# Kernel optimization log

Measured on AMD Instinct MI355X. Metric: run time of the kernel, lower is better.

## Reference

```python
import jax, jax.numpy as jnp
import numpy as np

N, E = 2048, 65536
EMBED, H0, H1 = 64, 128, 128
VOCAB = 625  # 5**k with k=4
SLOPE = 0.01  # F.leaky_relu_ default negative slope


def setup_inputs() -> dict:
    key = jax.random.key(0)
    ks = jax.random.split(key, 20)
    f = jax.random.normal
    return {
        "node_ids": jax.random.randint(ks[0], (N,), 0, VOCAB),
        "edge_index": jax.random.randint(ks[1], (2, E), 0, N),
        "edge_attr": jax.random.uniform(ks[2], (E, 1), dtype=jnp.float32),
        "m": (jax.random.uniform(ks[3], (N, N)) > 0.5).astype(jnp.float32),
        "emb": f(ks[4], (VOCAB, EMBED), dtype=jnp.float32) * 0.1,
        "l0_lin1": f(ks[5], (H0, EMBED + 1), dtype=jnp.float32) * 0.1,
        "l0_lin2": f(ks[6], (H0, H0), dtype=jnp.float32) * 0.1,
        "l0_att_l": f(ks[7], (H0,), dtype=jnp.float32) * 0.1,
        "l0_att_r": f(ks[8], (EMBED,), dtype=jnp.float32) * 0.1,
        "l0_bias": f(ks[9], (H0,), dtype=jnp.float32) * 0.1,
        "l1_lin1": f(ks[10], (H1, H0 + 1), dtype=jnp.float32) * 0.1,
        "l1_lin2": f(ks[11], (H1, H1), dtype=jnp.float32) * 0.1,
        "l1_att_l": f(ks[12], (H1,), dtype=jnp.float32) * 0.1,
        "l1_att_r": f(ks[13], (H0,), dtype=jnp.float32) * 0.1,
        "l1_bias": f(ks[14], (H1,), dtype=jnp.float32) * 0.1,
        "W1": f(ks[15], (20, (EMBED + H0 + H1) * 2), dtype=jnp.float32) * 0.1,
        "b1": f(ks[16], (20,), dtype=jnp.float32) * 0.1,
        "W2": f(ks[17], (20,), dtype=jnp.float32) * 0.1,
        "b2": f(ks[18], (1,), dtype=jnp.float32) * 0.1,
    }


def _segment_softmax(alpha, index, n):
    # numerically-stable softmax over edges grouped by destination node
    amax = jax.ops.segment_max(alpha, index, num_segments=n)
    amax = jnp.where(jnp.isfinite(amax), amax, 0.0)
    e = jnp.exp(alpha - amax[index])
    denom = jax.ops.segment_sum(e, index, num_segments=n)
    return e / (denom[index] + 1e-16)


def _gate_conv(x, src, dst, edge_attr, lin1, lin2, att_l, att_r, bias, n):
    # PyG AttentiveFP GATEConv: message = lin2(leaky_relu(lin1([x_j, e]))) * alpha
    h = jax.nn.leaky_relu(jnp.concatenate([x[src], edge_attr], axis=-1) @ lin1.T, SLOPE)  # [E,out]
    alpha = jax.nn.leaky_relu(h @ att_l + x[dst] @ att_r, SLOPE)  # [E]
    alpha = _segment_softmax(alpha, dst, n)
    msg = (h @ lin2.T) * alpha[:, None]
    return jax.ops.segment_sum(msg, dst, num_segments=n) + bias


def reference(node_ids, edge_index, edge_attr, m, emb,
              l0_lin1, l0_lin2, l0_att_l, l0_att_r, l0_bias,
              l1_lin1, l1_lin2, l1_att_l, l1_att_r, l1_bias,
              W1, b1, W2, b2):
    src, dst = edge_index[0], edge_index[1]
    x = emb[node_ids]  # [N, EMBED]
    h1 = jax.nn.relu(_gate_conv(x, src, dst, edge_attr, l0_lin1, l0_lin2, l0_att_l, l0_att_r, l0_bias, N))
    h2 = jax.nn.relu(_gate_conv(h1, src, dst, edge_attr, l1_lin1, l1_lin2, l1_att_l, l1_att_r, l1_bias, N))
    feat = jnp.concatenate([x, h1, h2], axis=-1)  # [N, C], C = EMBED+H0+H1
    C = feat.shape[-1]
    # 1x1 conv over concat([x_i, x_j]) == split linear: out[c,i,j] = W1[c,:C]@feat[i] + W1[c,C:]@feat[j] + b1[c]
    a = feat @ W1[:, :C].T  # [N, 20] row (i) term
    b = feat @ W1[:, C:].T  # [N, 20] col (j) term
    h = jax.nn.relu(a[:, None, :] + b[None, :, :] + b1)  # [N, N, 20]
    logits = (h @ W2 + b2[0]) * m  # [N, N]; mask multiplies logits as in original
    return jax.nn.softmax(logits, axis=1)
```

## Files before the change

kernel.cpp:

```cpp
#include <hip/hip_runtime.h>
#include <math.h>

#define N 2048
#define E 65536
#define EMBED 64
#define H 128
#define NT 20
#define C3 320
#define CAP 96
#define SLOPE 0.01f

__device__ __forceinline__ float leaky(float x) { return x > 0.f ? x : SLOPE * x; }

__device__ __forceinline__ float wave_sum(float v) {
#pragma unroll
    for (int o = 32; o > 0; o >>= 1) v += __shfl_xor(v, o, 64);
    return v;
}

__global__ __launch_bounds__(256) void k_scatprep(
    const int* __restrict__ ei, const float* __restrict__ eattr,
    int* __restrict__ cursor, int* __restrict__ srcs, float* __restrict__ eas,
    const float* __restrict__ l1_lin1, float* __restrict__ WT1,
    const float* __restrict__ l0_lin2, float* __restrict__ LT0,
    const float* __restrict__ l1_lin2, float* __restrict__ LT1,
    const int* __restrict__ ids, const float* __restrict__ emb,
    const float* __restrict__ l0_lin1,
    float* __restrict__ x, float* __restrict__ A) {
    int b = blockIdx.x;
    int tid = threadIdx.x;
    if (b < 256) {
        int e = b * 256 + tid;
        int d = ei[E + e];
        int pos = atomicAdd(&cursor[d], 1);
        if (pos < CAP) {
            srcs[d * CAP + pos] = ei[e];
            eas[d * CAP + pos] = eattr[e];
        }
    } else if (b < 448) {
        int j = (b - 256) * 256 + tid;
        if (j < 16384) {
            int c = j >> 7, k = j & 127;
            WT1[j] = l1_lin1[k * (H + 1) + c];
        } else if (j < 32768) {
            int jj = j - 16384; int c = jj >> 7, k = jj & 127;
            LT0[jj] = l0_lin2[k * H + c];
        } else {
            int jj = j - 32768; int c = jj >> 7, k = jj & 127;
            LT1[jj] = l1_lin2[k * H + c];
        }
    } else {
        __shared__ float lw[EMBED][130];
        int n0 = (b - 448) * 8;
        for (int j = tid; j < H * (EMBED + 1); j += 256) {
            int k = j / (EMBED + 1), c = j % (EMBED + 1);
            float v = l0_lin1[j];
            if (c < EMBED) lw[c][k] = v;
        }
        for (int idx = tid; idx < 8 * EMBED; idx += 256) {
            int g = idx >> 6, c = idx & 63;
            x[(n0 + g) * EMBED + c] = emb[ids[n0 + g] * EMBED + c];
        }
        __syncthreads();
        int k = tid & 127, half = tid >> 7;
        const float* xr[4];
#pragma unroll
        for (int it = 0; it < 4; it++) {
            int nn = __builtin_amdgcn_readfirstlane(n0 + 2 * it + half);
            xr[it] = emb + (size_t)ids[nn] * EMBED;
        }
        float acc[4] = {0.f, 0.f, 0.f, 0.f};
#pragma unroll 4
        for (int c = 0; c < EMBED; c++) {
            float wt = lw[c][k];
#pragma unroll
            for (int it = 0; it < 4; it++) acc[it] = fmaf(xr[it][c], wt, acc[it]);
        }
#pragma unroll
        for (int it = 0; it < 4; it++) A[(n0 + 2 * it + half) * H + k] = acc[it];
    }
}

__global__ __launch_bounds__(256) void k_gate(
    const float* __restrict__ xin, int D,
    const float* __restrict__ A,
    const float* __restrict__ lin1, int stride,
    const float* __restrict__ att_l, const float* __restrict__ att_r,
    const int* __restrict__ srcs, const float* __restrict__ eas,
    const int* __restrict__ cursor,
    float* __restrict__ agg) {
    int dst = blockIdx.x;
    int tid = threadIdx.x;
    int wv = tid >> 6, lane = tid & 63;

    float p = 0.f;
    for (int c = lane; c < D; c += 64) p += xin[dst * D + c] * att_r[c];
    float xr = wave_sum(p);

    int c0 = 2 * lane;
    float attl0 = att_l[c0], attl1 = att_l[c0 + 1];
    float w0 = lin1[c0 * stride + D];
    float w1 = lin1[(c0 + 1) * stride + D];

    int cnt = cursor[dst]; if (cnt > CAP) cnt = CAP;
    int base = dst * CAP;
    int end = base + cnt;
    float mmax = -INFINITY, s = 0.f, v0 = 0.f, v1 = 0.f;

    int i = base + wv;
    float ea = 0.f; float2 av = {0.f, 0.f};
    if (i < end) {
        int sn = srcs[i]; ea = eas[i];
        av = *(const float2*)&A[sn * H + c0];
    }
    while (i < end) {
        int i2 = i + 4;
        float ea2 = 0.f; float2 av2 = {0.f, 0.f};
        if (i2 < end) {
            int sn2 = srcs[i2]; ea2 = eas[i2];
            av2 = *(const float2*)&A[sn2 * H + c0];
        }
        float h0 = leaky(fmaf(w0, ea, av.x));
        float h1 = leaky(fmaf(w1, ea, av.y));
        float alpha = leaky(wave_sum(h0 * attl0 + h1 * attl1) + xr);
        float mnew = fmaxf(mmax, alpha);
        float scale = __expf(mmax - mnew);
        float wgt = __expf(alpha - mnew);
        s = fmaf(s, scale, wgt);
        v0 = fmaf(wgt, h0, v0 * scale);
        v1 = fmaf(wgt, h1, v1 * scale);
        mmax = mnew;
        i = i2; ea = ea2; av = av2;
    }

    __shared__ float msh[4], ssh[4], vsh[4][H];
    if (lane == 0) { msh[wv] = mmax; ssh[wv] = s; }
    *(float2*)&vsh[wv][c0] = make_float2(v0, v1);
    __syncthreads();
    if (tid < H) {
        float mM = fmaxf(fmaxf(msh[0], msh[1]), fmaxf(msh[2], msh[3]));
        float stot = 0.f, vtot = 0.f;
#pragma unroll
        for (int w = 0; w < 4; w++) {
            float sc = (ssh[w] > 0.f) ? __expf(msh[w] - mM) : 0.f;
            stot = fmaf(ssh[w], sc, stot);
            vtot = fmaf(vsh[w][tid], sc, vtot);
        }
        agg[dst * H + tid] = vtot / (stot + 1e-16f);
    }
}

__global__ __launch_bounds__(256) void k_lin1(const float* __restrict__ agg0,
                                              const float* __restrict__ LT0,
                                              const float* __restrict__ b0,
                                              const float* __restrict__ WT1,
                                              float* __restrict__ h1,
                                              float* __restrict__ A) {
    __shared__ float hs[8][H];
    int n0 = blockIdx.x * 8;
    int tid = threadIdx.x;
    int k = tid & 127, half = tid >> 7;
    const float* ar[4];
#pragma unroll
    for (int it = 0; it < 4; it++) {
        int nn = __builtin_amdgcn_readfirstlane(n0 + 2 * it + half);
        ar[it] = agg0 + (size_t)nn * H;
    }
    float bk = b0[k];
    float acc[4] = {bk, bk, bk, bk};
#pragma unroll 4
    for (int c = 0; c < H; c++) {
        float wt = LT0[c * H + k];
#pragma unroll
        for (int it = 0; it < 4; it++) acc[it] = fmaf(ar[it][c], wt, acc[it]);
    }
#pragma unroll
    for (int it = 0; it < 4; it++) {
        int g = 2 * it + half;
        float hv = fmaxf(acc[it], 0.f);
        h1[(n0 + g) * H + k] = hv;
        hs[g][k] = hv;
    }
    __syncthreads();
    float a2[4] = {0.f, 0.f, 0.f, 0.f};
#pragma unroll 2
    for (int ct = 0; ct < H / 4; ct++) {
        float w0 = WT1[(4 * ct + 0) * H + k];
        float w1 = WT1[(4 * ct + 1) * H + k];
        float w2 = WT1[(4 * ct + 2) * H + k];
        float w3 = WT1[(4 * ct + 3) * H + k];
#pragma unroll
        for (int it = 0; it < 4; it++) {
            float4 hv = *(const float4*)&hs[2 * it + half][4 * ct];
            a2[it] = fmaf(hv.x, w0, a2[it]);
            a2[it] = fmaf(hv.y, w1, a2[it]);
            a2[it] = fmaf(hv.z, w2, a2[it]);
            a2[it] = fmaf(hv.w, w3, a2[it]);
        }
    }
#pragma unroll
    for (int it = 0; it < 4; it++) A[(n0 + 2 * it + half) * H + k] = a2[it];
}

__global__ __launch_bounds__(256) void k_tail(const float* __restrict__ agg1,
                                              const float* __restrict__ LT1,
                                              const float* __restrict__ bL1,
                                              const float* __restrict__ x,
                                              const float* __restrict__ h1g,
                                              const float* __restrict__ W1,
                                              float* __restrict__ aArr,
                                              float* __restrict__ bT) {
    __shared__ float feat[8][C3];
    int n0 = blockIdx.x * 8;
    int tid = threadIdx.x;
    int k = tid & 127, half = tid >> 7;
    for (int idx = tid; idx < 8 * EMBED; idx += 256) {
        int g = idx >> 6, c = idx & 63;
        feat[g][c] = x[(n0 + g) * EMBED + c];
    }
    for (int idx = tid; idx < 8 * H; idx += 256) {
        int g = idx >> 7, c = idx & 127;
        feat[g][EMBED + c] = h1g[(n0 + g) * H + c];
    }
    const float* ar[4];
#pragma unroll
    for (int it = 0; it < 4; it++) {
        int nn = __builtin_amdgcn_readfirstlane(n0 + 2 * it + half);
        ar[it] = agg1 + (size_t)nn * H;
    }
    float bk = bL1[k];
    float acc[4] = {bk, bk, bk, bk};
#pragma unroll 4
    for (int c = 0; c < H; c++) {
        float wt = LT1[c * H + k];
#pragma unroll
        for (int it = 0; it < 4; it++) acc[it] = fmaf(ar[it][c], wt, acc[it]);
    }
#pragma unroll
    for (int it = 0; it < 4; it++)
        feat[2 * it + half][EMBED + H + k] = fmaxf(acc[it], 0.f);
    __syncthreads();
    for (int o = tid; o < 320; o += 256) {
        int g = o / 40, u = o % 40;
        int t = u % 20, side = u / 20;
        const float* wrow = W1 + t * (2 * C3) + side * C3;
        float s = 0.f;
#pragma unroll 4
        for (int ct = 0; ct < C3 / 4; ct++) {
            float4 fv = *(const float4*)&feat[g][4 * ct];
            float4 wv = *(const float4*)&wrow[4 * ct];
            s = fmaf(fv.x, wv.x, s);
            s = fmaf(fv.y, wv.y, s);
            s = fmaf(fv.z, wv.z, s);
            s = fmaf(fv.w, wv.w, s);
        }
        if (side == 0) aArr[(n0 + g) * NT + t] = s;
        else bT[t * N + (n0 + g)] = s;
    }
}

__global__ __launch_bounds__(256) void k_final(const float* __restrict__ aArr,
                                               const float* __restrict__ bT,
                                               const float* __restrict__ b1,
                                               const float* __restrict__ W2,
                                               const float* __restrict__ b2,
                                               const float* __restrict__ mmat,
                                               float* __restrict__ out) {
    __shared__ float lg[4][N];
    __shared__ float ash[4][NT];
    __shared__ float red[16];
    int i0 = blockIdx.x * 4;
    int tid = threadIdx.x;
    int wv = tid >> 6;
    if (tid < 4 * NT) ash[tid / NT][tid % NT] = aArr[i0 * NT + tid];
    float w2r[NT], b1r[NT];
#pragma unroll
    for (int t = 0; t < NT; t++) { w2r[t] = W2[t]; b1r[t] = b1[t]; }
    float b2v = b2[0];
    __syncthreads();

    float tmax[4] = {-INFINITY, -INFINITY, -INFINITY, -INFINITY};
    for (int j = tid; j < N; j += 256) {
        float bt[NT];
#pragma unroll
        for (int t = 0; t < NT; t++) bt[t] = bT[t * N + j];
#pragma unroll
        for (int g = 0; g < 4; g++) {
            float l = b2v;
#pragma unroll
            for (int t = 0; t < NT; t++)
                l += fmaxf(ash[g][t] + bt[t] + b1r[t], 0.f) * w2r[t];
            l *= mmat[(size_t)(i0 + g) * N + j];
            lg[g][j] = l;
            tmax[g] = fmaxf(tmax[g], l);
        }
    }
#pragma unroll
    for (int g = 0; g < 4; g++) {
#pragma unroll
        for (int o = 32; o > 0; o >>= 1) tmax[g] = fmaxf(tmax[g], __shfl_xor(tmax[g], o, 64));
    }
    if ((tid & 63) == 0) {
#pragma unroll
        for (int g = 0; g < 4; g++) red[wv * 4 + g] = tmax[g];
    }
    __syncthreads();
    float mfin[4];
#pragma unroll
    for (int g = 0; g < 4; g++)
        mfin[g] = fmaxf(fmaxf(red[g], red[4 + g]), fmaxf(red[8 + g], red[12 + g]));
    __syncthreads();

    float ts[4] = {0.f, 0.f, 0.f, 0.f};
    for (int j = tid; j < N; j += 256) {
#pragma unroll
        for (int g = 0; g < 4; g++) {
            float e = __expf(lg[g][j] - mfin[g]);
            lg[g][j] = e;
            ts[g] += e;
        }
    }
#pragma unroll
    for (int g = 0; g < 4; g++) {
#pragma unroll
        for (int o = 32; o > 0; o >>= 1) ts[g] += __shfl_xor(ts[g], o, 64);
    }
    if ((tid & 63) == 0) {
#pragma unroll
        for (int g = 0; g < 4; g++) red[wv * 4 + g] = ts[g];
    }
    __syncthreads();
    float inv[4];
#pragma unroll
    for (int g = 0; g < 4; g++)
        inv[g] = 1.f / (red[g] + red[4 + g] + red[8 + g] + red[12 + g]);

    for (int j = tid; j < N; j += 256) {
#pragma unroll
        for (int g = 0; g < 4; g++)
            out[(size_t)(i0 + g) * N + j] = lg[g][j] * inv[g];
    }
}

extern "C" void kernel_launch(void* const* d_in, const int* in_sizes, int n_in,
                              void* d_out, int out_size, void* d_ws, size_t ws_size,
                              hipStream_t stream) {
    const int*   node_ids = (const int*)d_in[0];
    const int*   ei       = (const int*)d_in[1];
    const float* eattr    = (const float*)d_in[2];
    const float* mmat     = (const float*)d_in[3];
    const float* emb      = (const float*)d_in[4];
    const float* l0_lin1  = (const float*)d_in[5];
    const float* l0_lin2  = (const float*)d_in[6];
    const float* l0_att_l = (const float*)d_in[7];
    const float* l0_att_r = (const float*)d_in[8];
    const float* l0_bias  = (const float*)d_in[9];
    const float* l1_lin1  = (const float*)d_in[10];
    const float* l1_lin2  = (const float*)d_in[11];
    const float* l1_att_l = (const float*)d_in[12];
    const float* l1_att_r = (const float*)d_in[13];
    const float* l1_bias  = (const float*)d_in[14];
    const float* W1       = (const float*)d_in[15];
    const float* b1       = (const float*)d_in[16];
    const float* W2       = (const float*)d_in[17];
    const float* b2       = (const float*)d_in[18];
    float* out = (float*)d_out;

    char* w = (char*)d_ws;
    auto alloc = [&](size_t bytes) {
        char* p = w;
        w += (bytes + 255) & ~(size_t)255;
        return p;
    };
    int*   cursor = (int*)alloc(N * sizeof(int));
    int*   srcs   = (int*)alloc(N * CAP * sizeof(int));
    float* eas    = (float*)alloc(N * CAP * sizeof(float));
    float* x      = (float*)alloc(N * EMBED * sizeof(float));
    float* A      = (float*)alloc(N * H * sizeof(float));
    float* agg    = (float*)alloc(N * H * sizeof(float));
    float* h1     = (float*)alloc(N * H * sizeof(float));
    float* aArr   = (float*)alloc(N * NT * sizeof(float));
    float* bT     = (float*)alloc(NT * N * sizeof(float));
    float* WT1    = (float*)alloc(H * H * sizeof(float));
    float* LT0    = (float*)alloc(H * H * sizeof(float));
    float* LT1    = (float*)alloc(H * H * sizeof(float));

    hipMemsetAsync(cursor, 0, N * sizeof(int), stream);

    k_scatprep<<<704, 256, 0, stream>>>(ei, eattr, cursor, srcs, eas,
                                        l1_lin1, WT1, l0_lin2, LT0, l1_lin2, LT1,
                                        node_ids, emb, l0_lin1, x, A);
    k_gate<<<N, 256, 0, stream>>>(x, EMBED, A, l0_lin1, EMBED + 1, l0_att_l, l0_att_r,
                                  srcs, eas, cursor, agg);
    k_lin1<<<N / 8, 256, 0, stream>>>(agg, LT0, l0_bias, WT1, h1, A);
    k_gate<<<N, 256, 0, stream>>>(h1, H, A, l1_lin1, H + 1, l1_att_l, l1_att_r,
                                  srcs, eas, cursor, agg);
    k_tail<<<N / 8, 256, 0, stream>>>(agg, LT1, l1_bias, x, h1, W1, aArr, bT);
    k_final<<<N / 4, 256, 0, stream>>>(aArr, bT, b1, W2, b2, mmat, out);
}
```

Baseline: 210.6 us.

## Fuse gate aggregation with following linear layers, one wave per destination node

```diff
diff --git a/kernel.cpp b/kernel.cpp
--- a/kernel.cpp
+++ b/kernel.cpp
@@ -18,7 +18,7 @@
     return v;
 }
 
-__global__ __launch_bounds__(256) void k_scatprep(
+__global__ __launch_bounds__(256) void k_prep(
     const int* __restrict__ ei, const float* __restrict__ eattr,
     int* __restrict__ cursor, int* __restrict__ srcs, float* __restrict__ eas,
     const float* __restrict__ l1_lin1, float* __restrict__ WT1,
@@ -81,178 +81,192 @@
     }
 }
 
-__global__ __launch_bounds__(256) void k_gate(
-    const float* __restrict__ xin, int D,
+__device__ __forceinline__ void gate_wave(
+    int dst, int lane, float xr,
     const float* __restrict__ A,
-    const float* __restrict__ lin1, int stride,
+    float w0, float w1, float attl0, float attl1,
+    const int* __restrict__ srcs, const float* __restrict__ eas, int cnt,
+    float& out0, float& out1) {
+    int c0 = 2 * lane;
+    int base = dst * CAP;
+    float mmax = -INFINITY, s = 0.f, v0 = 0.f, v1 = 0.f;
+    for (int i0 = 0; i0 < cnt; i0 += 8) {
+        int nb = cnt - i0; if (nb > 8) nb = 8;
+        float h0[8], h1[8], p[8];
+#pragma unroll
+        for (int e = 0; e < 8; e++) {
+            float ea = 0.f; float2 av = make_float2(0.f, 0.f);
+            if (e < nb) {
+                int sn = srcs[base + i0 + e];
+                ea = eas[base + i0 + e];
+                av = *(const float2*)&A[sn * H + c0];
+            }
+            h0[e] = leaky(fmaf(w0, ea, av.x));
+            h1[e] = leaky(fmaf(w1, ea, av.y));
+            p[e] = h0[e] * attl0 + h1[e] * attl1;
+        }
+#pragma unroll
+        for (int o = 32; o > 0; o >>= 1) {
+#pragma unroll
+            for (int e = 0; e < 8; e++) p[e] += __shfl_xor(p[e], o, 64);
+        }
+        float alpha[8];
+#pragma unroll
+        for (int e = 0; e < 8; e++)
+            alpha[e] = (e < nb) ? leaky(p[e] + xr) : -INFINITY;
+        float mb = alpha[0];
+#pragma unroll
+        for (int e = 1; e < 8; e++) mb = fmaxf(mb, alpha[e]);
+        float mnew = fmaxf(mmax, mb);
+        float scale = __expf(mmax - mnew);
+        float sw = 0.f, sv0 = 0.f, sv1 = 0.f;
+#pragma unroll
+        for (int e = 0; e < 8; e++) {
+            float we = __expf(alpha[e] - mnew);
+            sw += we;
+            sv0 = fmaf(we, h0[e], sv0);
+            sv1 = fmaf(we, h1[e], sv1);
+        }
+        s = fmaf(s, scale, sw);
+        v0 = fmaf(v0, scale, sv0);
+        v1 = fmaf(v1, scale, sv1);
+        mmax = mnew;
+    }
+    float inv = 1.f / (s + 1e-16f);
+    out0 = v0 * inv;
+    out1 = v1 * inv;
+}
+
+__global__ __launch_bounds__(512) void k_g0(
+    const float* __restrict__ x, const float* __restrict__ A0,
+    const float* __restrict__ l0_lin1,
     const float* __restrict__ att_l, const float* __restrict__ att_r,
     const int* __restrict__ srcs, const float* __restrict__ eas,
     const int* __restrict__ cursor,
-    float* __restrict__ agg) {
-    int dst = blockIdx.x;
-    int tid = threadIdx.x;
-    int wv = tid >> 6, lane = tid & 63;
-
-    float p = 0.f;
-    for (int c = lane; c < D; c += 64) p += xin[dst * D + c] * att_r[c];
-    float xr = wave_sum(p);
-
-    int c0 = 2 * lane;
-    float attl0 = att_l[c0], attl1 = att_l[c0 + 1];
-    float w0 = lin1[c0 * stride + D];
-    float w1 = lin1[(c0 + 1) * stride + D];
-
-    int cnt = cursor[dst]; if (cnt > CAP) cnt = CAP;
-    int base = dst * CAP;
-    int end = base + cnt;
-    float mmax = -INFINITY, s = 0.f, v0 = 0.f, v1 = 0.f;
-
-    int i = base + wv;
-    float ea = 0.f; float2 av = {0.f, 0.f};
-    if (i < end) {
-        int sn = srcs[i]; ea = eas[i];
-        av = *(const float2*)&A[sn * H + c0];
-    }
-    while (i < end) {
-        int i2 = i + 4;
-        float ea2 = 0.f; float2 av2 = {0.f, 0.f};
-        if (i2 < end) {
-            int sn2 = srcs[i2]; ea2 = eas[i2];
-            av2 = *(const float2*)&A[sn2 * H + c0];
-        }
-        float h0 = leaky(fmaf(w0, ea, av.x));
-        float h1 = leaky(fmaf(w1, ea, av.y));
-        float alpha = leaky(wave_sum(h0 * attl0 + h1 * attl1) + xr);
-        float mnew = fmaxf(mmax, alpha);
-        float scale = __expf(mmax - mnew);
-        float wgt = __expf(alpha - mnew);
-        s = fmaf(s, scale, wgt);
-        v0 = fmaf(wgt, h0, v0 * scale);
-        v1 = fmaf(wgt, h1, v1 * scale);
-        mmax = mnew;
-        i = i2; ea = ea2; av = av2;
-    }
-
-    __shared__ float msh[4], ssh[4], vsh[4][H];
-    if (lane == 0) { msh[wv] = mmax; ssh[wv] = s; }
-    *(float2*)&vsh[wv][c0] = make_float2(v0, v1);
-    __syncthreads();
-    if (tid < H) {
-        float mM = fmaxf(fmaxf(msh[0], msh[1]), fmaxf(msh[2], msh[3]));
-        float stot = 0.f, vtot = 0.f;
-#pragma unroll
-        for (int w = 0; w < 4; w++) {
-            float sc = (ssh[w] > 0.f) ? __expf(msh[w] - mM) : 0.f;
-            stot = fmaf(ssh[w], sc, stot);
-            vtot = fmaf(vsh[w][tid], sc, vtot);
-        }
-        agg[dst * H + tid] = vtot / (stot + 1e-16f);
-    }
-}
-
-__global__ __launch_bounds__(256) void k_lin1(const float* __restrict__ agg0,
-                                              const float* __restrict__ LT0,
-                                              const float* __restrict__ b0,
-                                              const float* __restrict__ WT1,
-                                              float* __restrict__ h1,
-                                              float* __restrict__ A) {
+    const float* __restrict__ LT0, const float* __restrict__ b0,
+    const float* __restrict__ WT1,
+    float* __restrict__ h1, float* __restrict__ A1) {
+    __shared__ float agg_s[8][H];
     __shared__ float hs[8][H];
     int n0 = blockIdx.x * 8;
     int tid = threadIdx.x;
-    int k = tid & 127, half = tid >> 7;
-    const float* ar[4];
-#pragma unroll
-    for (int it = 0; it < 4; it++) {
-        int nn = __builtin_amdgcn_readfirstlane(n0 + 2 * it + half);
-        ar[it] = agg0 + (size_t)nn * H;
-    }
+    int wv = __builtin_amdgcn_readfirstlane(tid >> 6);
+    int lane = tid & 63;
+    int c0 = 2 * lane;
+
+    int dst = n0 + wv;
+    float xr = wave_sum(x[dst * EMBED + lane] * att_r[lane]);
+    float attl0 = att_l[c0], attl1 = att_l[c0 + 1];
+    float w0 = l0_lin1[c0 * (EMBED + 1) + EMBED];
+    float w1 = l0_lin1[(c0 + 1) * (EMBED + 1) + EMBED];
+    int cnt = cursor[dst]; if (cnt > CAP) cnt = CAP;
+
+    float o0, o1;
+    gate_wave(dst, lane, xr, A0, w0, w1, attl0, attl1, srcs, eas, cnt, o0, o1);
+    agg_s[wv][c0] = o0;
+    agg_s[wv][c0 + 1] = o1;
+    __syncthreads();
+
+    int k = tid & 127, q = tid >> 7;
     float bk = b0[k];
-    float acc[4] = {bk, bk, bk, bk};
+    float acc0 = bk, acc1 = bk;
 #pragma unroll 4
     for (int c = 0; c < H; c++) {
         float wt = LT0[c * H + k];
-#pragma unroll
-        for (int it = 0; it < 4; it++) acc[it] = fmaf(ar[it][c], wt, acc[it]);
-    }
-#pragma unroll
-    for (int it = 0; it < 4; it++) {
-        int g = 2 * it + half;
-        float hv = fmaxf(acc[it], 0.f);
-        h1[(n0 + g) * H + k] = hv;
-        hs[g][k] = hv;
-    }
-    __syncthreads();
-    float a2[4] = {0.f, 0.f, 0.f, 0.f};
+        acc0 = fmaf(agg_s[q][c], wt, acc0);
+        acc1 = fmaf(agg_s[q + 4][c], wt, acc1);
+    }
+    float hv0 = fmaxf(acc0, 0.f), hv1 = fmaxf(acc1, 0.f);
+    h1[(n0 + q) * H + k] = hv0;
+    h1[(n0 + q + 4) * H + k] = hv1;
+    hs[q][k] = hv0;
+    hs[q + 4][k] = hv1;
+    __syncthreads();
+
+    float a0 = 0.f, a1 = 0.f;
 #pragma unroll 2
     for (int ct = 0; ct < H / 4; ct++) {
-        float w0 = WT1[(4 * ct + 0) * H + k];
-        float w1 = WT1[(4 * ct + 1) * H + k];
-        float w2 = WT1[(4 * ct + 2) * H + k];
-        float w3 = WT1[(4 * ct + 3) * H + k];
-#pragma unroll
-        for (int it = 0; it < 4; it++) {
-            float4 hv = *(const float4*)&hs[2 * it + half][4 * ct];
-            a2[it] = fmaf(hv.x, w0, a2[it]);
-            a2[it] = fmaf(hv.y, w1, a2[it]);
-            a2[it] = fmaf(hv.z, w2, a2[it]);
-            a2[it] = fmaf(hv.w, w3, a2[it]);
-        }
-    }
-#pragma unroll
-    for (int it = 0; it < 4; it++) A[(n0 + 2 * it + half) * H + k] = a2[it];
-}
-
-__global__ __launch_bounds__(256) void k_tail(const float* __restrict__ agg1,
-                                              const float* __restrict__ LT1,
-                                              const float* __restrict__ bL1,
-                                              const float* __restrict__ x,
-                                              const float* __restrict__ h1g,
-                                              const float* __restrict__ W1,
-                                              float* __restrict__ aArr,
-                                              float* __restrict__ bT) {
+        float u0 = WT1[(4 * ct + 0) * H + k];
+        float u1 = WT1[(4 * ct + 1) * H + k];
+        float u2 = WT1[(4 * ct + 2) * H + k];
+        float u3 = WT1[(4 * ct + 3) * H + k];
+        float4 f0 = *(const float4*)&hs[q][4 * ct];
+        float4 f1 = *(const float4*)&hs[q + 4][4 * ct];
+        a0 = fmaf(f0.x, u0, a0); a0 = fmaf(f0.y, u1, a0);
+        a0 = fmaf(f0.z, u2, a0); a0 = fmaf(f0.w, u3, a0);
+        a1 = fmaf(f1.x, u0, a1); a1 = fmaf(f1.y, u1, a1);
+        a1 = fmaf(f1.z, u2, a1); a1 = fmaf(f1.w, u3, a1);
+    }
+    A1[(n0 + q) * H + k] = a0;
+    A1[(n0 + q + 4) * H + k] = a1;
+}
+
+__global__ __launch_bounds__(512) void k_g1(
+    const float* __restrict__ h1g, const float* __restrict__ A1,
+    const float* __restrict__ l1_lin1,
+    const float* __restrict__ att_l, const float* __restrict__ att_r,
+    const int* __restrict__ srcs, const float* __restrict__ eas,
+    const int* __restrict__ cursor,
+    const float* __restrict__ LT1, const float* __restrict__ bL1,
+    const float* __restrict__ x, const float* __restrict__ W1,
+    float* __restrict__ aArr, float* __restrict__ bT) {
+    __shared__ float agg_s[8][H];
     __shared__ float feat[8][C3];
     int n0 = blockIdx.x * 8;
     int tid = threadIdx.x;
-    int k = tid & 127, half = tid >> 7;
-    for (int idx = tid; idx < 8 * EMBED; idx += 256) {
+    int wv = __builtin_amdgcn_readfirstlane(tid >> 6);
+    int lane = tid & 63;
+    int c0 = 2 * lane;
+
+    int dst = n0 + wv;
+    float xr = wave_sum(h1g[dst * H + lane] * att_r[lane] +
+                        h1g[dst * H + 64 + lane] * att_r[64 + lane]);
+    float attl0 = att_l[c0], attl1 = att_l[c0 + 1];
+    float w0 = l1_lin1[c0 * (H + 1) + H];
+    float w1 = l1_lin1[(c0 + 1) * (H + 1) + H];
+    int cnt = cursor[dst]; if (cnt > CAP) cnt = CAP;
+
+    float o0, o1;
+    gate_wave(dst, lane, xr, A1, w0, w1, attl0, attl1, srcs, eas, cnt, o0, o1);
+    agg_s[wv][c0] = o0;
+    agg_s[wv][c0 + 1] = o1;
+
+    for (int idx = tid; idx < 8 * EMBED; idx += 512) {
         int g = idx >> 6, c = idx & 63;
         feat[g][c] = x[(n0 + g) * EMBED + c];
     }
-    for (int idx = tid; idx < 8 * H; idx += 256) {
+    for (int idx = tid; idx < 8 * H; idx += 512) {
         int g = idx >> 7, c = idx & 127;
         feat[g][EMBED + c] = h1g[(n0 + g) * H + c];
     }
-    const float* ar[4];
-#pragma unroll
-    for (int it = 0; it < 4; it++) {
-        int nn = __builtin_amdgcn_readfirstlane(n0 + 2 * it + half);
-        ar[it] = agg1 + (size_t)nn * H;
-    }
+    __syncthreads();
+
+    int k = tid & 127, q = tid >> 7;
     float bk = bL1[k];
-    float acc[4] = {bk, bk, bk, bk};
+    float acc0 = bk, acc1 = bk;
 #pragma unroll 4
     for (int c = 0; c < H; c++) {
         float wt = LT1[c * H + k];
-#pragma unroll
-        for (int it = 0; it < 4; it++) acc[it] = fmaf(ar[it][c], wt, acc[it]);
-    }
-#pragma unroll
-    for (int it = 0; it < 4; it++)
-        feat[2 * it + half][EMBED + H + k] = fmaxf(acc[it], 0.f);
-    __syncthreads();
-    for (int o = tid; o < 320; o += 256) {
-        int g = o / 40, u = o % 40;
+        acc0 = fmaf(agg_s[q][c], wt, acc0);
+        acc1 = fmaf(agg_s[q + 4][c], wt, acc1);
+    }
+    feat[q][EMBED + H + k] = fmaxf(acc0, 0.f);
+    feat[q + 4][EMBED + H + k] = fmaxf(acc1, 0.f);
+    __syncthreads();
+
+    if (tid < 320) {
+        int g = tid / 40, u = tid % 40;
         int t = u % 20, side = u / 20;
         const float* wrow = W1 + t * (2 * C3) + side * C3;
         float s = 0.f;
 #pragma unroll 4
         for (int ct = 0; ct < C3 / 4; ct++) {
             float4 fv = *(const float4*)&feat[g][4 * ct];
-            float4 wv = *(const float4*)&wrow[4 * ct];
-            s = fmaf(fv.x, wv.x, s);
-            s = fmaf(fv.y, wv.y, s);
-            s = fmaf(fv.z, wv.z, s);
-            s = fmaf(fv.w, wv.w, s);
+            float4 wv4 = *(const float4*)&wrow[4 * ct];
+            s = fmaf(fv.x, wv4.x, s);
+            s = fmaf(fv.y, wv4.y, s);
+            s = fmaf(fv.z, wv4.z, s);
+            s = fmaf(fv.w, wv4.w, s);
         }
         if (side == 0) aArr[(n0 + g) * NT + t] = s;
         else bT[t * N + (n0 + g)] = s;
@@ -376,8 +390,8 @@
     int*   srcs   = (int*)alloc(N * CAP * sizeof(int));
     float* eas    = (float*)alloc(N * CAP * sizeof(float));
     float* x      = (float*)alloc(N * EMBED * sizeof(float));
-    float* A      = (float*)alloc(N * H * sizeof(float));
-    float* agg    = (float*)alloc(N * H * sizeof(float));
+    float* A0     = (float*)alloc(N * H * sizeof(float));
+    float* A1     = (float*)alloc(N * H * sizeof(float));
     float* h1     = (float*)alloc(N * H * sizeof(float));
     float* aArr   = (float*)alloc(N * NT * sizeof(float));
     float* bT     = (float*)alloc(NT * N * sizeof(float));
@@ -387,14 +401,12 @@
 
     hipMemsetAsync(cursor, 0, N * sizeof(int), stream);
 
-    k_scatprep<<<704, 256, 0, stream>>>(ei, eattr, cursor, srcs, eas,
-                                        l1_lin1, WT1, l0_lin2, LT0, l1_lin2, LT1,
-                                        node_ids, emb, l0_lin1, x, A);
-    k_gate<<<N, 256, 0, stream>>>(x, EMBED, A, l0_lin1, EMBED + 1, l0_att_l, l0_att_r,
-                                  srcs, eas, cursor, agg);
-    k_lin1<<<N / 8, 256, 0, stream>>>(agg, LT0, l0_bias, WT1, h1, A);
-    k_gate<<<N, 256, 0, stream>>>(h1, H, A, l1_lin1, H + 1, l1_att_l, l1_att_r,
-                                  srcs, eas, cursor, agg);
-    k_tail<<<N / 8, 256, 0, stream>>>(agg, LT1, l1_bias, x, h1, W1, aArr, bT);
+    k_prep<<<704, 256, 0, stream>>>(ei, eattr, cursor, srcs, eas,
+                                    l1_lin1, WT1, l0_lin2, LT0, l1_lin2, LT1,
+                                    node_ids, emb, l0_lin1, x, A0);
+    k_g0<<<N / 8, 512, 0, stream>>>(x, A0, l0_lin1, l0_att_l, l0_att_r,
+                                    srcs, eas, cursor, LT0, l0_bias, WT1, h1, A1);
+    k_g1<<<N / 8, 512, 0, stream>>>(h1, A1, l1_lin1, l1_att_l, l1_att_r,
+                                    srcs, eas, cursor, LT1, l1_bias, x, W1, aArr, bT);
     k_final<<<N / 4, 256, 0, stream>>>(aArr, bT, b1, W2, b2, mmat, out);
 }
```

Measured after the change: 193.8 us. 8.0% less time.
